# Kernel tuning notes

Measured on AMD Instinct MI355X. Metric: run time of the kernel, lower is better.

The kernel has to match this reference:

```python
import jax, jax.numpy as jnp
import numpy as np

N_NODES = 100000
N_EDGES = 1000000
D_FEAT = 64
N_GRAPHS = 64


def setup_inputs() -> dict:
    key = jax.random.key(0)
    ks = jax.random.split(key, 5)
    x = jax.random.normal(ks[0], (N_NODES, D_FEAT), dtype=jnp.float32)
    edge_index = jax.random.randint(ks[1], (2, N_EDGES), 0, N_NODES, dtype=jnp.int32)
    batch = jnp.sort(jax.random.randint(ks[2], (N_NODES,), 0, N_GRAPHS, dtype=jnp.int32))
    s = 1.0 / np.sqrt(D_FEAT)
    W1 = jax.random.uniform(ks[3], (D_FEAT, D_FEAT), jnp.float32, -s, s)
    W2 = jax.random.uniform(ks[4], (D_FEAT, D_FEAT), jnp.float32, -s, s)
    b1 = jnp.zeros((D_FEAT,), jnp.float32)
    b2 = jnp.zeros((D_FEAT,), jnp.float32)
    return {"x": x, "edge_index": edge_index, "batch": batch,
            "W1": W1, "b1": b1, "W2": W2, "b2": b2}


def gcn_conv(x, edge_index, W, b, num_nodes):
    # PyG GCNConv: h = D^{-1/2} (A + I) D^{-1/2} (x W) + b
    loops = jnp.arange(num_nodes, dtype=edge_index.dtype)
    row = jnp.concatenate([edge_index[0], loops])  # source nodes
    col = jnp.concatenate([edge_index[1], loops])  # target nodes
    h = x @ W  # [N, D]
    deg = jax.ops.segment_sum(jnp.ones_like(col, dtype=h.dtype), col,
                              num_segments=num_nodes)  # >= 1 due to self loops
    dinv = jax.lax.rsqrt(deg)
    norm = dinv[row] * dinv[col]  # [E+N]
    out = jax.ops.segment_sum(h[row] * norm[:, None], col, num_segments=num_nodes)
    return out + b


def reference(x, edge_index, batch, W1, b1, W2, b2):
    n = x.shape[0]
    h = gcn_conv(x, edge_index, W1, b1, n)
    h = gcn_conv(h, edge_index, W2, b2, n)
    # global_mean_pool over graph ids
    sums = jax.ops.segment_sum(h, batch, num_segments=N_GRAPHS)  # [G, D]
    cnts = jax.ops.segment_sum(jnp.ones((n, 1), h.dtype), batch,
                               num_segments=N_GRAPHS)
    return sums / jnp.maximum(cnts, 1.0)
```

## Files before the change

### kernel.cpp

```cpp
#include <hip/hip_runtime.h>
#include <hip/hip_fp16.h>

#define DFEAT 64
#define NG 64
#define TILE 128
#define NBLK 256
#define NBMAX 1024

__global__ __launch_bounds__(256) void k_cnt(const int* __restrict__ col,
                                             int* __restrict__ cnt_m,
                                             int e, int nb, int chunk) {
  __shared__ int hist[NBMAX];
  int tid = threadIdx.x;
  int blk = blockIdx.x;
  for (int b = tid; b < nb; b += 256) hist[b] = 0;
  __syncthreads();
  int lo = blk * chunk, hi = min(lo + chunk, e);
  for (int i = lo + tid; i < hi; i += 256)
    atomicAdd(&hist[col[i] >> 7], 1);
  __syncthreads();
  for (int b = tid; b < nb; b += 256)
    cnt_m[(size_t)blk * nb + b] = hist[b];
}

__global__ __launch_bounds__(256) void k_colscan(int* __restrict__ cnt_m,
                                                 int* __restrict__ gcount, int nb) {
  __shared__ int sh[256];
  int tid = threadIdx.x;
  int b = blockIdx.x;
  int v = cnt_m[(size_t)tid * nb + b];
  sh[tid] = v;
  __syncthreads();
  for (int off = 1; off < 256; off <<= 1) {
    int t = (tid >= off) ? sh[tid - off] : 0;
    __syncthreads();
    sh[tid] += t;
    __syncthreads();
  }
  cnt_m[(size_t)tid * nb + b] = sh[tid] - v;
  if (tid == 255) gcount[b] = sh[255];
}

__global__ __launch_bounds__(1024) void k_bscan(const int* __restrict__ gcount,
                                                int* __restrict__ base, int nb) {
  __shared__ int sh[1024];
  int tid = threadIdx.x;
  int v = (tid < nb) ? gcount[tid] : 0;
  sh[tid] = v;
  __syncthreads();
  for (int off = 1; off < 1024; off <<= 1) {
    int t = (tid >= off) ? sh[tid - off] : 0;
    __syncthreads();
    sh[tid] += t;
    __syncthreads();
  }
  if (tid < nb) base[tid] = sh[tid] - v;
  if (tid == 0) base[nb] = sh[1023];
}

__global__ __launch_bounds__(256) void k_bin2(const int* __restrict__ row,
                                              const int* __restrict__ col,
                                              const int* __restrict__ base,
                                              const int* __restrict__ cnt_m,
                                              int* __restrict__ pairs,
                                              int e, int nb, int chunk) {
  __shared__ int gl[NBMAX];
  __shared__ int lcur[NBMAX];
  int tid = threadIdx.x;
  int blk = blockIdx.x;
  for (int b = tid; b < nb; b += 256) {
    gl[b] = base[b] + cnt_m[(size_t)blk * nb + b];
    lcur[b] = 0;
  }
  __syncthreads();
  int lo = blk * chunk, hi = min(lo + chunk, e);
  for (int i = lo + tid; i < hi; i += 256) {
    int s = row[i], t = col[i];
    int b = t >> 7;
    int pos = gl[b] + atomicAdd(&lcur[b], 1);
    pairs[pos] = s | ((t & (TILE - 1)) << 20);
  }
}

__global__ __launch_bounds__(256) void k_csr(const int* __restrict__ pairs,
                                             const int* __restrict__ base,
                                             int* __restrict__ starts,
                                             int* __restrict__ srcs,
                                             float* __restrict__ dinv,
                                             int n, int e) {
  __shared__ int cnt[TILE];
  __shared__ int cur[TILE];
  __shared__ int sc[TILE];
  int tid = threadIdx.x;
  int b = blockIdx.x;
  int tile0 = b * TILE;
  if (tid < TILE) cnt[tid] = 0;
  __syncthreads();
  int e0 = base[b], e1 = base[b + 1];
  for (int i = e0 + tid; i < e1; i += 256)
    atomicAdd(&cnt[(unsigned)pairs[i] >> 20], 1);
  __syncthreads();
  int c = (tid < TILE) ? cnt[tid] : 0;
  if (tid < TILE) sc[tid] = c;
  __syncthreads();
  for (int off = 1; off < TILE; off <<= 1) {
    int t = (tid < TILE && tid >= off) ? sc[tid - off] : 0;
    __syncthreads();
    if (tid < TILE) sc[tid] += t;
    __syncthreads();
  }
  if (tid < TILE) {
    int excl = sc[tid] - c;
    cur[tid] = excl;
    int node = tile0 + tid;
    if (node < n) {
      starts[node] = e0 + excl;
      dinv[node] = rsqrtf(1.0f + (float)c);
    }
  }
  if (b == 0 && tid == 0) starts[n] = e;
  __syncthreads();
  for (int i = e0 + tid; i < e1; i += 256) {
    int p = pairs[i];
    int pos = atomicAdd(&cur[(unsigned)p >> 20], 1);
    srcs[e0 + pos] = p & 0xFFFFF;
  }
}

__global__ __launch_bounds__(256) void k_xs(const float* __restrict__ x,
                                            const float* __restrict__ dinv,
                                            __half2* __restrict__ xh, int n32) {
  int i = blockIdx.x * 256 + threadIdx.x;
  if (i < n32) {
    float2 v = ((const float2*)x)[i];
    float d = dinv[i >> 5];
    xh[i] = __floats2half2_rn(v.x * d, v.y * d);
  }
}

__global__ __launch_bounds__(256) void k_w12(const float* __restrict__ W1,
                                             const float* __restrict__ W2,
                                             const float* __restrict__ b1,
                                             float* __restrict__ WW,
                                             float* __restrict__ bw) {
  __shared__ float w1[4096], w2[4096];
  int tid = threadIdx.x;
  for (int i = tid; i < 4096; i += 256) { w1[i] = W1[i]; w2[i] = W2[i]; }
  __syncthreads();
  for (int p = tid; p < 4096; p += 256) {
    int k = p >> 6, d = p & 63;
    float a = 0.f;
    for (int m = 0; m < 64; ++m) a += w1[k * 64 + m] * w2[m * 64 + d];
    WW[p] = a;
  }
  if (tid < 64) {
    float a = 0.f;
    for (int k = 0; k < 64; ++k) a += b1[k] * w2[k * 64 + tid];
    bw[tid] = a;
  }
}

__device__ __forceinline__ void acc8(float2& a0, float2& a1, float2& a2,
                                     float2& a3, float4 v) {
  const __half2* hp = (const __half2*)&v;
  float2 t;
  t = __half22float2(hp[0]); a0.x += t.x; a0.y += t.y;
  t = __half22float2(hp[1]); a1.x += t.x; a1.y += t.y;
  t = __half22float2(hp[2]); a2.x += t.x; a2.y += t.y;
  t = __half22float2(hp[3]); a3.x += t.x; a3.y += t.y;
}

__global__ __launch_bounds__(256) void k_gather1(const int* __restrict__ starts,
                                                 const int* __restrict__ srcs,
                                                 const float* __restrict__ dinv,
                                                 const __half2* __restrict__ xh,
                                                 __half2* __restrict__ z1h,
                                                 float* __restrict__ u, int n) {
  int node = blockIdx.x * 32 + (threadIdx.x >> 3);
  if (node >= n) return;
  int l = threadIdx.x & 7;
  int s = starts[node];
  int deg = starts[node + 1] - s;
  float dc = dinv[node];
  const float4* xf = (const float4*)xh;
  float4 sv = xf[(size_t)node * 8 + l];
  float2 a0 = make_float2(0.f, 0.f), a1 = a0, a2 = a0, a3 = a0;
  acc8(a0, a1, a2, a3, sv);
  float wsum = 0.f;
  int j = 0;
  for (; j + 3 < deg; j += 4) {
    int r0 = srcs[s + j + 0];
    int r1 = srcs[s + j + 1];
    int r2 = srcs[s + j + 2];
    int r3 = srcs[s + j + 3];
    float4 v0 = xf[(size_t)r0 * 8 + l];
    float4 v1 = xf[(size_t)r1 * 8 + l];
    float4 v2 = xf[(size_t)r2 * 8 + l];
    float4 v3 = xf[(size_t)r3 * 8 + l];
    wsum += dinv[r0] + dinv[r1] + dinv[r2] + dinv[r3];
    acc8(a0, a1, a2, a3, v0);
    acc8(a0, a1, a2, a3, v1);
    acc8(a0, a1, a2, a3, v2);
    acc8(a0, a1, a2, a3, v3);
  }
  for (; j < deg; ++j) {
    int r = srcs[s + j];
    float4 v = xf[(size_t)r * 8 + l];
    wsum += dinv[r];
    acc8(a0, a1, a2, a3, v);
  }
  float s2 = dc * dc;
  float4 ov;
  __half2* op = (__half2*)&ov;
  op[0] = __floats2half2_rn(s2 * a0.x, s2 * a0.y);
  op[1] = __floats2half2_rn(s2 * a1.x, s2 * a1.y);
  op[2] = __floats2half2_rn(s2 * a2.x, s2 * a2.y);
  op[3] = __floats2half2_rn(s2 * a3.x, s2 * a3.y);
  ((float4*)z1h)[(size_t)node * 8 + l] = ov;
  if (l == 0) u[node] = dc * (dc + wsum);
}

__global__ __launch_bounds__(256) void k_gather2(const int* __restrict__ starts,
                                                 const int* __restrict__ srcs,
                                                 const float* __restrict__ dinv,
                                                 const __half2* __restrict__ z1h,
                                                 float* __restrict__ z2, int n) {
  int node = blockIdx.x * 32 + (threadIdx.x >> 3);
  if (node >= n) return;
  int l = threadIdx.x & 7;
  int s = starts[node];
  int deg = starts[node + 1] - s;
  float dc = dinv[node];
  const float4* xf = (const float4*)z1h;
  float4 sv = xf[(size_t)node * 8 + l];
  float2 a0 = make_float2(0.f, 0.f), a1 = a0, a2 = a0, a3 = a0;
  acc8(a0, a1, a2, a3, sv);
  int j = 0;
  for (; j + 3 < deg; j += 4) {
    int r0 = srcs[s + j + 0];
    int r1 = srcs[s + j + 1];
    int r2 = srcs[s + j + 2];
    int r3 = srcs[s + j + 3];
    float4 v0 = xf[(size_t)r0 * 8 + l];
    float4 v1 = xf[(size_t)r1 * 8 + l];
    float4 v2 = xf[(size_t)r2 * 8 + l];
    float4 v3 = xf[(size_t)r3 * 8 + l];
    acc8(a0, a1, a2, a3, v0);
    acc8(a0, a1, a2, a3, v1);
    acc8(a0, a1, a2, a3, v2);
    acc8(a0, a1, a2, a3, v3);
  }
  for (; j < deg; ++j) {
    int r = srcs[s + j];
    float4 v = xf[(size_t)r * 8 + l];
    acc8(a0, a1, a2, a3, v);
  }
  float4* zr = (float4*)(z2 + (size_t)node * 64);
  zr[l * 2 + 0] = make_float4(dc * a0.x, dc * a0.y, dc * a1.x, dc * a1.y);
  zr[l * 2 + 1] = make_float4(dc * a2.x, dc * a2.y, dc * a3.x, dc * a3.y);
}

__global__ void k_pool2(const float* __restrict__ z2, const float* __restrict__ u,
                        const int* __restrict__ batch, float* __restrict__ S,
                        float* __restrict__ T, float* __restrict__ cntf, int n) {
  int d = threadIdx.x;
  int start = blockIdx.x * 64;
  if (start >= n) return;
  int end = min(start + 64, n);
  int curg = batch[start];
  float acc = 0.f, cnt = 0.f, ua = 0.f;
  for (int i = start; i < end; ++i) {
    int g = batch[i];
    if (g != curg) {
      unsafeAtomicAdd(&S[curg * 64 + d], acc);
      if (d == 0) {
        unsafeAtomicAdd(&cntf[curg], cnt);
        unsafeAtomicAdd(&T[curg], ua);
      }
      acc = 0.f; cnt = 0.f; ua = 0.f;
      curg = g;
    }
    acc += z2[(size_t)i * 64 + d];
    if (d == 0) { cnt += 1.f; ua += u[i]; }
  }
  unsafeAtomicAdd(&S[curg * 64 + d], acc);
  if (d == 0) {
    unsafeAtomicAdd(&cntf[curg], cnt);
    unsafeAtomicAdd(&T[curg], ua);
  }
}

__global__ __launch_bounds__(256) void k_final2(const float* __restrict__ S,
                                                const float* __restrict__ T,
                                                const float* __restrict__ cntf,
                                                const float* __restrict__ WW,
                                                const float* __restrict__ bw,
                                                const float* __restrict__ b2,
                                                float* __restrict__ out) {
  __shared__ float sS[4096], sW[4096];
  int tid = threadIdx.x;
  for (int i = tid; i < 4096; i += 256) { sS[i] = S[i]; sW[i] = WW[i]; }
  __syncthreads();
  for (int p = tid; p < 4096; p += 256) {
    int g = p >> 6, d = p & 63;
    float a = 0.f;
    for (int k = 0; k < 64; ++k) a += sS[g * 64 + k] * sW[k * 64 + d];
    float c = fmaxf(cntf[g], 1.0f);
    out[p] = (a + T[g] * bw[d]) / c + b2[d];
  }
}

extern "C" void kernel_launch(void* const* d_in, const int* in_sizes, int n_in,
                              void* d_out, int out_size, void* d_ws, size_t ws_size,
                              hipStream_t stream) {
  const float* x = (const float*)d_in[0];
  const int* ei = (const int*)d_in[1];
  const int* bat = (const int*)d_in[2];
  const float* W1 = (const float*)d_in[3];
  const float* b1 = (const float*)d_in[4];
  const float* W2 = (const float*)d_in[5];
  const float* b2 = (const float*)d_in[6];
  float* out = (float*)d_out;

  int n = in_sizes[0] / 64;
  int e = in_sizes[1] / 2;
  const int* rowp = ei;
  const int* colp = ei + e;
  int nb = (n + TILE - 1) / TILE;
  int chunk = (e + NBLK - 1) / NBLK;

  char* ws = (char*)d_ws;
  size_t off = 0;
  auto alloc = [&](size_t elems) {
    void* p = ws + off;
    off += ((elems * 4 + 255) & ~(size_t)255);
    return p;
  };
  float* S = (float*)alloc(NG * DFEAT);
  float* cntf = (float*)alloc(NG);
  float* T = (float*)alloc(NG);
  size_t zbytes = off;
  int* gcount = (int*)alloc(nb);
  int* base = (int*)alloc(nb + 1);
  int* cnt_m = (int*)alloc((size_t)NBLK * nb);
  float* dinv = (float*)alloc(n);
  int* starts = (int*)alloc(n + 1);
  int* srcs = (int*)alloc(e);
  float* u = (float*)alloc(n);
  float* WW = (float*)alloc(DFEAT * DFEAT);
  float* bw = (float*)alloc(DFEAT);
  __half2* xh = (__half2*)alloc((size_t)n * 32);
  __half2* z1h = (__half2*)alloc((size_t)n * 32);
  float* z2 = (float*)alloc((size_t)n * 64);
  int* pairs = (int*)z2;

  int nbw = (n + 31) / 32;
  int n32 = n * 32;

  hipMemsetAsync(S, 0, zbytes, stream);
  k_cnt<<<NBLK, 256, 0, stream>>>(colp, cnt_m, e, nb, chunk);
  k_colscan<<<nb, 256, 0, stream>>>(cnt_m, gcount, nb);
  k_bscan<<<1, 1024, 0, stream>>>(gcount, base, nb);
  k_bin2<<<NBLK, 256, 0, stream>>>(rowp, colp, base, cnt_m, pairs, e, nb, chunk);
  k_csr<<<nb, 256, 0, stream>>>(pairs, base, starts, srcs, dinv, n, e);
  k_xs<<<(n32 + 255) / 256, 256, 0, stream>>>(x, dinv, xh, n32);
  k_w12<<<1, 256, 0, stream>>>(W1, W2, b1, WW, bw);

  k_gather1<<<nbw, 256, 0, stream>>>(starts, srcs, dinv, xh, z1h, u, n);
  k_gather2<<<nbw, 256, 0, stream>>>(starts, srcs, dinv, z1h, z2, n);

  k_pool2<<<(n + 63) / 64, 64, 0, stream>>>(z2, u, bat, S, T, cntf, n);
  k_final2<<<1, 256, 0, stream>>>(S, T, cntf, WW, bw, b2, out);
}
```

Before: 214.3 us.

## Fuse x scaling into CSR build and pooling into gather kernels

Folds the fp16 prescaling of x into the per-tile CSR kernel, and fuses the global mean pool into the gather kernels. The gathers now reduce per-node results across the wavefront when all nodes share one graph id, and atomically add them into replicated per-graph accumulators, which the final kernel sums. Graph counts come from binary searches on the sorted batch array instead of a pooling pass. This removes the fp32 z2 round trip, the u buffer and two launches, at the cost of atomics contention and relying on batch being sorted.

```diff
diff --git a/kernel.cpp b/kernel.cpp
--- a/kernel.cpp
+++ b/kernel.cpp
@@ -6,6 +6,7 @@
 #define TILE 128
 #define NBLK 256
 #define NBMAX 1024
+#define NREP 16
 
 __global__ __launch_bounds__(256) void k_cnt(const int* __restrict__ col,
                                              int* __restrict__ cnt_m,
@@ -84,13 +85,16 @@
 
 __global__ __launch_bounds__(256) void k_csr(const int* __restrict__ pairs,
                                              const int* __restrict__ base,
+                                             const float* __restrict__ x,
                                              int* __restrict__ starts,
                                              int* __restrict__ srcs,
                                              float* __restrict__ dinv,
+                                             __half2* __restrict__ xh,
                                              int n, int e) {
   __shared__ int cnt[TILE];
   __shared__ int cur[TILE];
   __shared__ int sc[TILE];
+  __shared__ float sdv[TILE];
   int tid = threadIdx.x;
   int b = blockIdx.x;
   int tile0 = b * TILE;
@@ -113,9 +117,11 @@
     int excl = sc[tid] - c;
     cur[tid] = excl;
     int node = tile0 + tid;
+    float d = rsqrtf(1.0f + (float)c);
+    sdv[tid] = (node < n) ? d : 0.f;
     if (node < n) {
       starts[node] = e0 + excl;
-      dinv[node] = rsqrtf(1.0f + (float)c);
+      dinv[node] = d;
     }
   }
   if (b == 0 && tid == 0) starts[n] = e;
@@ -125,27 +131,41 @@
     int pos = atomicAdd(&cur[(unsigned)p >> 20], 1);
     srcs[e0 + pos] = p & 0xFFFFF;
   }
-}
-
-__global__ __launch_bounds__(256) void k_xs(const float* __restrict__ x,
-                                            const float* __restrict__ dinv,
-                                            __half2* __restrict__ xh, int n32) {
-  int i = blockIdx.x * 256 + threadIdx.x;
-  if (i < n32) {
-    float2 v = ((const float2*)x)[i];
-    float d = dinv[i >> 5];
-    xh[i] = __floats2half2_rn(v.x * d, v.y * d);
+  int nnode = min(n - tile0, TILE);
+  if (nnode > 0) {
+    int nfl = nnode * 16;
+    const float4* xf = (const float4*)(x + (size_t)tile0 * 64);
+    float2* xo = (float2*)xh + (size_t)tile0 * 16;
+    for (int p = tid; p < nfl; p += 256) {
+      float4 v = xf[p];
+      float d = sdv[p >> 4];
+      float2 st;
+      ((__half2*)&st)[0] = __floats2half2_rn(v.x * d, v.y * d);
+      ((__half2*)&st)[1] = __floats2half2_rn(v.z * d, v.w * d);
+      xo[p] = st;
+    }
   }
 }
 
 __global__ __launch_bounds__(256) void k_w12(const float* __restrict__ W1,
                                              const float* __restrict__ W2,
                                              const float* __restrict__ b1,
+                                             const int* __restrict__ batch,
                                              float* __restrict__ WW,
-                                             float* __restrict__ bw) {
+                                             float* __restrict__ bw,
+                                             float* __restrict__ cntf, int n) {
   __shared__ float w1[4096], w2[4096];
   int tid = threadIdx.x;
   for (int i = tid; i < 4096; i += 256) { w1[i] = W1[i]; w2[i] = W2[i]; }
+  if (tid < NG) {
+    int g = tid;
+    int lo = 0, hi = n;
+    while (lo < hi) { int m = (lo + hi) >> 1; if (batch[m] < g) lo = m + 1; else hi = m; }
+    int a = lo;
+    lo = 0; hi = n;
+    while (lo < hi) { int m = (lo + hi) >> 1; if (batch[m] < g + 1) lo = m + 1; else hi = m; }
+    cntf[g] = (float)(lo - a);
+  }
   __syncthreads();
   for (int p = tid; p < 4096; p += 256) {
     int k = p >> 6, d = p & 63;
@@ -174,16 +194,22 @@
                                                  const int* __restrict__ srcs,
                                                  const float* __restrict__ dinv,
                                                  const __half2* __restrict__ xh,
+                                                 const int* __restrict__ batch,
                                                  __half2* __restrict__ z1h,
-                                                 float* __restrict__ u, int n) {
-  int node = blockIdx.x * 32 + (threadIdx.x >> 3);
-  if (node >= n) return;
-  int l = threadIdx.x & 7;
-  int s = starts[node];
-  int deg = starts[node + 1] - s;
-  float dc = dinv[node];
+                                                 float* __restrict__ Tr, int n) {
+  int tid = threadIdx.x;
+  int node = blockIdx.x * 32 + (tid >> 3);
+  bool act = node < n;
+  int nc = act ? node : n - 1;
+  int l = tid & 7;
+  int lane = tid & 63;
+  int rep = blockIdx.x & (NREP - 1);
+  int s = starts[nc];
+  int deg = act ? (starts[nc + 1] - s) : 0;
+  float dc = dinv[nc];
+  int g = batch[nc];
   const float4* xf = (const float4*)xh;
-  float4 sv = xf[(size_t)node * 8 + l];
+  float4 sv = xf[(size_t)nc * 8 + l];
   float2 a0 = make_float2(0.f, 0.f), a1 = a0, a2 = a0, a3 = a0;
   acc8(a0, a1, a2, a3, sv);
   float wsum = 0.f;
@@ -209,30 +235,49 @@
     wsum += dinv[r];
     acc8(a0, a1, a2, a3, v);
   }
-  float s2 = dc * dc;
-  float4 ov;
-  __half2* op = (__half2*)&ov;
-  op[0] = __floats2half2_rn(s2 * a0.x, s2 * a0.y);
-  op[1] = __floats2half2_rn(s2 * a1.x, s2 * a1.y);
-  op[2] = __floats2half2_rn(s2 * a2.x, s2 * a2.y);
-  op[3] = __floats2half2_rn(s2 * a3.x, s2 * a3.y);
-  ((float4*)z1h)[(size_t)node * 8 + l] = ov;
-  if (l == 0) u[node] = dc * (dc + wsum);
+  if (act) {
+    float s2 = dc * dc;
+    float4 ov;
+    __half2* op = (__half2*)&ov;
+    op[0] = __floats2half2_rn(s2 * a0.x, s2 * a0.y);
+    op[1] = __floats2half2_rn(s2 * a1.x, s2 * a1.y);
+    op[2] = __floats2half2_rn(s2 * a2.x, s2 * a2.y);
+    op[3] = __floats2half2_rn(s2 * a3.x, s2 * a3.y);
+    ((float4*)z1h)[(size_t)node * 8 + l] = ov;
+  }
+  float uval = act ? dc * (dc + wsum) : 0.f;
+  int g0 = __shfl(g, 0);
+  bool uni = (__all(g == g0) != 0);
+  if (!uni) {
+    if (act && l == 0) unsafeAtomicAdd(&Tr[rep * NG + g], uval);
+  } else {
+    float uv = (l == 0) ? uval : 0.f;
+    uv += __shfl_xor(uv, 8);
+    uv += __shfl_xor(uv, 16);
+    uv += __shfl_xor(uv, 32);
+    if (lane == 0 && uv != 0.f) unsafeAtomicAdd(&Tr[rep * NG + g0], uv);
+  }
 }
 
 __global__ __launch_bounds__(256) void k_gather2(const int* __restrict__ starts,
                                                  const int* __restrict__ srcs,
                                                  const float* __restrict__ dinv,
                                                  const __half2* __restrict__ z1h,
-                                                 float* __restrict__ z2, int n) {
-  int node = blockIdx.x * 32 + (threadIdx.x >> 3);
-  if (node >= n) return;
-  int l = threadIdx.x & 7;
-  int s = starts[node];
-  int deg = starts[node + 1] - s;
-  float dc = dinv[node];
+                                                 const int* __restrict__ batch,
+                                                 float* __restrict__ Sr, int n) {
+  int tid = threadIdx.x;
+  int node = blockIdx.x * 32 + (tid >> 3);
+  bool act = node < n;
+  int nc = act ? node : n - 1;
+  int l = tid & 7;
+  int lane = tid & 63;
+  int rep = blockIdx.x & (NREP - 1);
+  int s = starts[nc];
+  int deg = act ? (starts[nc + 1] - s) : 0;
+  float dc = dinv[nc];
+  int g = batch[nc];
   const float4* xf = (const float4*)z1h;
-  float4 sv = xf[(size_t)node * 8 + l];
+  float4 sv = xf[(size_t)nc * 8 + l];
   float2 a0 = make_float2(0.f, 0.f), a1 = a0, a2 = a0, a3 = a0;
   acc8(a0, a1, a2, a3, sv);
   int j = 0;
@@ -255,58 +300,66 @@
     float4 v = xf[(size_t)r * 8 + l];
     acc8(a0, a1, a2, a3, v);
   }
-  float4* zr = (float4*)(z2 + (size_t)node * 64);
-  zr[l * 2 + 0] = make_float4(dc * a0.x, dc * a0.y, dc * a1.x, dc * a1.y);
-  zr[l * 2 + 1] = make_float4(dc * a2.x, dc * a2.y, dc * a3.x, dc * a3.y);
-}
-
-__global__ void k_pool2(const float* __restrict__ z2, const float* __restrict__ u,
-                        const int* __restrict__ batch, float* __restrict__ S,
-                        float* __restrict__ T, float* __restrict__ cntf, int n) {
-  int d = threadIdx.x;
-  int start = blockIdx.x * 64;
-  if (start >= n) return;
-  int end = min(start + 64, n);
-  int curg = batch[start];
-  float acc = 0.f, cnt = 0.f, ua = 0.f;
-  for (int i = start; i < end; ++i) {
-    int g = batch[i];
-    if (g != curg) {
-      unsafeAtomicAdd(&S[curg * 64 + d], acc);
-      if (d == 0) {
-        unsafeAtomicAdd(&cntf[curg], cnt);
-        unsafeAtomicAdd(&T[curg], ua);
-      }
-      acc = 0.f; cnt = 0.f; ua = 0.f;
-      curg = g;
+  float f[8];
+  f[0] = act ? dc * a0.x : 0.f;
+  f[1] = act ? dc * a0.y : 0.f;
+  f[2] = act ? dc * a1.x : 0.f;
+  f[3] = act ? dc * a1.y : 0.f;
+  f[4] = act ? dc * a2.x : 0.f;
+  f[5] = act ? dc * a2.y : 0.f;
+  f[6] = act ? dc * a3.x : 0.f;
+  f[7] = act ? dc * a3.y : 0.f;
+  int g0 = __shfl(g, 0);
+  bool uni = (__all(g == g0) != 0);
+  if (!uni) {
+    if (act) {
+#pragma unroll
+      for (int k = 0; k < 8; ++k)
+        unsafeAtomicAdd(&Sr[(size_t)rep * 4096 + g * 64 + l * 8 + k], f[k]);
     }
-    acc += z2[(size_t)i * 64 + d];
-    if (d == 0) { cnt += 1.f; ua += u[i]; }
-  }
-  unsafeAtomicAdd(&S[curg * 64 + d], acc);
-  if (d == 0) {
-    unsafeAtomicAdd(&cntf[curg], cnt);
-    unsafeAtomicAdd(&T[curg], ua);
-  }
-}
-
-__global__ __launch_bounds__(256) void k_final2(const float* __restrict__ S,
-                                                const float* __restrict__ T,
+  } else {
+#pragma unroll
+    for (int k = 0; k < 8; ++k) {
+      f[k] += __shfl_xor(f[k], 8);
+      f[k] += __shfl_xor(f[k], 16);
+      f[k] += __shfl_xor(f[k], 32);
+    }
+    if (lane < 8) {
+#pragma unroll
+      for (int k = 0; k < 8; ++k)
+        if (f[k] != 0.f)
+          unsafeAtomicAdd(&Sr[(size_t)rep * 4096 + g0 * 64 + lane * 8 + k], f[k]);
+    }
+  }
+}
+
+__global__ __launch_bounds__(256) void k_final2(const float* __restrict__ Sr,
+                                                const float* __restrict__ Tr,
                                                 const float* __restrict__ cntf,
                                                 const float* __restrict__ WW,
                                                 const float* __restrict__ bw,
                                                 const float* __restrict__ b2,
                                                 float* __restrict__ out) {
-  __shared__ float sS[4096], sW[4096];
-  int tid = threadIdx.x;
-  for (int i = tid; i < 4096; i += 256) { sS[i] = S[i]; sW[i] = WW[i]; }
+  __shared__ float sS[4096], sW[4096], sT[64];
+  int tid = threadIdx.x;
+  for (int i = tid; i < 4096; i += 256) {
+    float a = 0.f;
+    for (int r = 0; r < NREP; ++r) a += Sr[(size_t)r * 4096 + i];
+    sS[i] = a;
+    sW[i] = WW[i];
+  }
+  if (tid < 64) {
+    float t = 0.f;
+    for (int r = 0; r < NREP; ++r) t += Tr[r * NG + tid];
+    sT[tid] = t;
+  }
   __syncthreads();
   for (int p = tid; p < 4096; p += 256) {
     int g = p >> 6, d = p & 63;
     float a = 0.f;
     for (int k = 0; k < 64; ++k) a += sS[g * 64 + k] * sW[k * 64 + d];
     float c = fmaxf(cntf[g], 1.0f);
-    out[p] = (a + T[g] * bw[d]) / c + b2[d];
+    out[p] = (a + sT[g] * bw[d]) / c + b2[d];
   }
 }
 
@@ -336,9 +389,9 @@
     off += ((elems * 4 + 255) & ~(size_t)255);
     return p;
   };
-  float* S = (float*)alloc(NG * DFEAT);
+  float* Sr = (float*)alloc((size_t)NREP * NG * DFEAT);
+  float* Tr = (float*)alloc(NREP * NG);
   float* cntf = (float*)alloc(NG);
-  float* T = (float*)alloc(NG);
   size_t zbytes = off;
   int* gcount = (int*)alloc(nb);
   int* base = (int*)alloc(nb + 1);
@@ -346,29 +399,24 @@
   float* dinv = (float*)alloc(n);
   int* starts = (int*)alloc(n + 1);
   int* srcs = (int*)alloc(e);
-  float* u = (float*)alloc(n);
   float* WW = (float*)alloc(DFEAT * DFEAT);
   float* bw = (float*)alloc(DFEAT);
   __half2* xh = (__half2*)alloc((size_t)n * 32);
   __half2* z1h = (__half2*)alloc((size_t)n * 32);
-  float* z2 = (float*)alloc((size_t)n * 64);
-  int* pairs = (int*)z2;
+  int* pairs = (int*)alloc(e);
 
   int nbw = (n + 31) / 32;
-  int n32 = n * 32;
-
-  hipMemsetAsync(S, 0, zbytes, stream);
+
+  hipMemsetAsync(Sr, 0, zbytes, stream);
   k_cnt<<<NBLK, 256, 0, stream>>>(colp, cnt_m, e, nb, chunk);
   k_colscan<<<nb, 256, 0, stream>>>(cnt_m, gcount, nb);
   k_bscan<<<1, 1024, 0, stream>>>(gcount, base, nb);
   k_bin2<<<NBLK, 256, 0, stream>>>(rowp, colp, base, cnt_m, pairs, e, nb, chunk);
-  k_csr<<<nb, 256, 0, stream>>>(pairs, base, starts, srcs, dinv, n, e);
-  k_xs<<<(n32 + 255) / 256, 256, 0, stream>>>(x, dinv, xh, n32);
-  k_w12<<<1, 256, 0, stream>>>(W1, W2, b1, WW, bw);
-
-  k_gather1<<<nbw, 256, 0, stream>>>(starts, srcs, dinv, xh, z1h, u, n);
-  k_gather2<<<nbw, 256, 0, stream>>>(starts, srcs, dinv, z1h, z2, n);
-
-  k_pool2<<<(n + 63) / 64, 64, 0, stream>>>(z2, u, bat, S, T, cntf, n);
-  k_final2<<<1, 256, 0, stream>>>(S, T, cntf, WW, bw, b2, out);
-}
+  k_csr<<<nb, 256, 0, stream>>>(pairs, base, x, starts, srcs, dinv, xh, n, e);
+  k_w12<<<1, 256, 0, stream>>>(W1, W2, b1, bat, WW, bw, cntf, n);
+
+  k_gather1<<<nbw, 256, 0, stream>>>(starts, srcs, dinv, xh, bat, z1h, Tr, n);
+  k_gather2<<<nbw, 256, 0, stream>>>(starts, srcs, dinv, z1h, bat, Sr, n);
+
+  k_final2<<<1, 256, 0, stream>>>(Sr, Tr, cntf, WW, bw, b2, out);
+}
```

Result: slower. 252.7 us (+17.9%).
